# Kernel optimization log

Measured on AMD Instinct MI355X. Metric: run time of the kernel, lower is better.

Reference implementation:

```python
import jax, jax.numpy as jnp
import numpy as np

K_TOP = 32
TEMPERATURE = 0.1
EPS = 1e-12  # torch F.normalize eps


def _l2_normalize(x):
    n = jnp.linalg.norm(x, axis=-1, keepdims=True)
    return x / jnp.maximum(n, EPS)


def setup_inputs() -> dict:
    key = jax.random.key(0)
    kq, kk, kv = jax.random.split(key, 3)
    B, T, d_k, d_v, N = 4, 512, 512, 512, 65536
    queries = jax.random.normal(kq, (B, T, d_k), dtype=jnp.float32)
    keys = jax.random.normal(kk, (N, d_k), dtype=jnp.float32)
    values = jax.random.normal(kv, (N, d_v), dtype=jnp.float32)
    return {"queries": queries, "keys": keys, "values": values}


def reference(queries, keys, values):
    B, T, d_k = queries.shape
    d_v = values.shape[1]
    flat_q = queries.reshape(B * T, d_k)
    qn = _l2_normalize(flat_q)           # [BT, d_k]
    kn = _l2_normalize(keys)             # [N, d_k]
    scores = qn @ kn.T                   # [BT, N] cosine similarities
    topk_scores, topk_idx = jax.lax.top_k(scores, K_TOP)  # [BT, K]
    attn = jax.nn.softmax(topk_scores / TEMPERATURE, axis=-1)  # [BT, K]
    retrieved = values[topk_idx]         # [BT, K, d_v]
    aggregated = jnp.einsum('nk,nkd->nd', attn, retrieved)  # [BT, d_v]
    return (aggregated.reshape(B, T, d_v),
            attn.reshape(B, T, K_TOP),
            topk_idx.reshape(B, T, K_TOP))
```

## Files before the change

kernel.cpp:

```cpp
#include <hip/hip_runtime.h>
#include <math.h>

#define M_ROWS 2048
#define N_KEYS 65536
#define DKK 512
#define DVV 512
#define KTOP 32
#define NSPLIT 16
#define NRANGE (N_KEYS / NSPLIT)
#define BM 128
#define BN 128
#define MBLKS (M_ROWS / BM)
#define NTILES (NRANGE / BN)
#define KSTEPS (DKK / 32)
#define TOT (NTILES * KSTEPS)
#define CAP 16
#define CSTR 17

typedef _Float16 f16x8 __attribute__((ext_vector_type(8)));
typedef _Float16 f16x4v __attribute__((ext_vector_type(4)));
typedef float f32x4 __attribute__((ext_vector_type(4)));


__device__ __forceinline__ void split4(const float4 v, float inv,
                                       _Float16* ph, _Float16* pl) {
  f16x4v h, l;
  float y;
  y = v.x * inv; h[0] = (_Float16)y; l[0] = (_Float16)(y - (float)h[0]);
  y = v.y * inv; h[1] = (_Float16)y; l[1] = (_Float16)(y - (float)h[1]);
  y = v.z * inv; h[2] = (_Float16)y; l[2] = (_Float16)(y - (float)h[2]);
  y = v.w * inv; h[3] = (_Float16)y; l[3] = (_Float16)(y - (float)h[3]);
  *(f16x4v*)ph = h; *(f16x4v*)pl = l;
}

__global__ void __launch_bounds__(256) norm_split_kernel(
    const float* __restrict__ q, const float* __restrict__ keys,
    _Float16* __restrict__ Qh, _Float16* __restrict__ Ql,
    _Float16* __restrict__ Kh, _Float16* __restrict__ Kl) {
  const int gw = (blockIdx.x * 256 + threadIdx.x) >> 6;
  const int lane = threadIdx.x & 63;
  const float* row; _Float16 *oh, *ol;
  if (gw < M_ROWS) {
    row = q + (size_t)gw * DKK; oh = Qh + (size_t)gw * DKK; ol = Ql + (size_t)gw * DKK;
  } else {
    const int n = gw - M_ROWS;
    if (n >= N_KEYS) return;
    row = keys + (size_t)n * DKK; oh = Kh + (size_t)n * DKK; ol = Kl + (size_t)n * DKK;
  }
  const float4 a = ((const float4*)row)[lane];
  const float4 b = ((const float4*)row)[lane + 64];
  float s = a.x*a.x + a.y*a.y + a.z*a.z + a.w*a.w
          + b.x*b.x + b.y*b.y + b.z*b.z + b.w*b.w;
#pragma unroll
  for (int off = 32; off; off >>= 1) s += __shfl_xor(s, off);
  const float inv = 1.0f / fmaxf(sqrtf(s), 1e-12f);
  split4(a, inv, oh + lane * 4,       ol + lane * 4);
  split4(b, inv, oh + 256 + lane * 4, ol + 256 + lane * 4);
}

__device__ __forceinline__ void insert32(float* tS, int* tI, float s, int idx) {
  const float ms = tS[31]; const int mi_ = tI[31];
  if (s < ms || (s == ms && idx > mi_)) return;
  int p = 0;
  while (p < KTOP && (tS[p] > s || (tS[p] == s && tI[p] < idx))) ++p;
  for (int qq = KTOP - 1; qq > p; --qq) { tS[qq] = tS[qq-1]; tI[qq] = tI[qq-1]; }
  tS[p] = s; tI[p] = idx;
}

__device__ __forceinline__ void gll16(const _Float16* g, _Float16* l) {
  __builtin_amdgcn_global_load_lds(
      (const __attribute__((address_space(1))) void*)g,
      (__attribute__((address_space(3))) void*)l, 16, 0, 0);
}

#define STAGE(B, N0V, KOF) do {                                  \
  const size_t _qa = qsrc + (size_t)(KOF);                       \
  const size_t _ba = (size_t)(N0V) * DKK + bsrc + (size_t)(KOF); \
  gll16(Qh + _qa, &stA[B][0][ldsA]);                             \
  gll16(Ql + _qa, &stA[B][1][ldsA]);                             \
  gll16(Kh + _ba, &stB[B][0][ldsA]);                             \
  gll16(Kl + _ba, &stB[B][1][ldsA]);                             \
} while (0)

#define KBAR(NVM) do {                                           \
  __builtin_amdgcn_sched_barrier(0);                             \
  asm volatile("s_waitcnt vmcnt(" #NVM ")" ::: "memory");        \
  __builtin_amdgcn_sched_barrier(0);                             \
  __builtin_amdgcn_s_barrier();                                  \
  __builtin_amdgcn_sched_barrier(0);                             \
} while (0)

#define LBAR() do {                                              \
  __builtin_amdgcn_sched_barrier(0);                             \
  asm volatile("s_waitcnt lgkmcnt(0)" ::: "memory");             \
  __builtin_amdgcn_sched_barrier(0);                             \
  __builtin_amdgcn_s_barrier();                                  \
  __builtin_amdgcn_sched_barrier(0);                             \
} while (0)

__global__ void __launch_bounds__(512, 2) gemm_topk_kernel(
    const _Float16* __restrict__ Qh, const _Float16* __restrict__ Ql,
    const _Float16* __restrict__ Kh, const _Float16* __restrict__ Kl,
    float* __restrict__ pscore, int* __restrict__ pidx) {
  __shared__ __attribute__((aligned(16))) _Float16 stA[3][2][BM * 32];
  __shared__ __attribute__((aligned(16))) _Float16 stB[3][2][BN * 32];
  __shared__ float topS[BM * 33];
  __shared__ int   topI[BM * 33];
  __shared__ float candS[BM * CSTR];
  __shared__ int   candI[BM * CSTR];
  __shared__ float mS[BM];
  __shared__ int   cnt[BM];
  __shared__ int   sOver;

  const int tid  = threadIdx.x;
  const int lane = tid & 63;
  const int w    = tid >> 6;
  const int wr   = w >> 1, wc = w & 1;
  const int cl   = lane & 15;
  const int g    = lane >> 4;
  const int g4   = g * 4;

  const int lin   = (int)(blockIdx.x + gridDim.x * blockIdx.y);
  const int virt  = (lin & 7) * 32 + (lin >> 3);
  const int mblk  = virt & (MBLKS - 1);
  const int split = virt >> 4;
  const int qbase  = mblk * BM;
  const int nbase0 = split * NRANGE;

  const int soct = (tid & 3) ^ ((tid >> 3) & 3);
  const int ldsA = tid * 8;
  const size_t qsrc = (size_t)(qbase + (tid >> 2)) * DKK + (size_t)soct * 8;
  const size_t bsrc = (size_t)(tid >> 2) * DKK + (size_t)soct * 8;

  int offA[2], offB[4];
#pragma unroll
  for (int mi = 0; mi < 2; ++mi) {
    const int r = wr * 32 + mi * 16 + cl;
    offA[mi] = r * 32 + (g ^ ((r >> 1) & 3)) * 8;
  }
#pragma unroll
  for (int ni = 0; ni < 4; ++ni) {
    const int c = wc * 64 + ni * 16 + cl;
    offB[ni] = c * 32 + (g ^ ((c >> 1) & 3)) * 8;
  }

  if (tid < BM) {
    mS[tid] = -INFINITY; cnt[tid] = 0;
#pragma unroll
    for (int j = 0; j < KTOP; ++j) { topS[tid*33+j] = -INFINITY; topI[tid*33+j] = 0x7fffffff; }
  }
  if (tid == 0) sOver = 0;

  STAGE(0, nbase0, 0);
  STAGE(1, nbase0, 32);

  int cur = 0;

  for (int ct = 0; ct < NTILES; ++ct) {
    const int n0 = nbase0 + ct * BN;
    f32x4 acc[2][4];
#pragma unroll
    for (int mi = 0; mi < 2; ++mi)
#pragma unroll
      for (int ni = 0; ni < 4; ++ni) acc[mi][ni] = (f32x4)0.0f;

    for (int ks = 0; ks < KSTEPS; ++ks) {
      const int s = ct * KSTEPS + ks;
      if (s == TOT - 1) { KBAR(0); } else { KBAR(4); }

      if (s + 2 < TOT) {
        int b2 = cur + 2; if (b2 >= 3) b2 -= 3;
        const int s2 = s + 2;
        const int ct2 = s2 >> 4, ks2 = s2 & 15;
        STAGE(b2, nbase0 + ct2 * BN, ks2 * 32);
      }

      f16x8 Ah[2], Al[2], Bh[4], Bl[4];
#pragma unroll
      for (int mi = 0; mi < 2; ++mi) {
        Ah[mi] = *(const f16x8*)&stA[cur][0][offA[mi]];
        Al[mi] = *(const f16x8*)&stA[cur][1][offA[mi]];
      }
#pragma unroll
      for (int ni = 0; ni < 4; ++ni) {
        Bh[ni] = *(const f16x8*)&stB[cur][0][offB[ni]];
        Bl[ni] = *(const f16x8*)&stB[cur][1][offB[ni]];
      }
      __builtin_amdgcn_s_setprio(1);
#pragma unroll
      for (int mi = 0; mi < 2; ++mi)
#pragma unroll
        for (int ni = 0; ni < 4; ++ni) {
          acc[mi][ni] = __builtin_amdgcn_mfma_f32_16x16x32_f16(Al[mi], Bh[ni], acc[mi][ni], 0, 0, 0);
          acc[mi][ni] = __builtin_amdgcn_mfma_f32_16x16x32_f16(Ah[mi], Bl[ni], acc[mi][ni], 0, 0, 0);
          acc[mi][ni] = __builtin_amdgcn_mfma_f32_16x16x32_f16(Ah[mi], Bh[ni], acc[mi][ni], 0, 0, 0);
        }
      __builtin_amdgcn_s_setprio(0);

      ++cur; if (cur >= 3) cur -= 3;
    }

    LBAR();
    float m[2][4];
#pragma unroll
    for (int mi = 0; mi < 2; ++mi) {
      const f32x4 mv = *(const f32x4*)&mS[wr * 32 + mi * 16 + g4];
      m[mi][0] = mv[0]; m[mi][1] = mv[1]; m[mi][2] = mv[2]; m[mi][3] = mv[3];
    }
    unsigned int pend = 0u;
#pragma unroll
    for (int mi = 0; mi < 2; ++mi)
#pragma unroll
      for (int ni = 0; ni < 4; ++ni)
#pragma unroll
        for (int j = 0; j < 4; ++j)
          if (acc[mi][ni][j] >= m[mi][j])
            pend |= 1u << (mi * 16 + ni * 4 + j);

    for (;;) {
      if (pend) {
#pragma unroll
        for (int mi = 0; mi < 2; ++mi)
#pragma unroll
          for (int ni = 0; ni < 4; ++ni)
#pragma unroll
            for (int j = 0; j < 4; ++j) {
              const int bit = mi * 16 + ni * 4 + j;
              if (pend & (1u << bit)) {
                const int r = wr * 32 + mi * 16 + g4 + j;
                const int t = atomicAdd(&cnt[r], 1);
                if (t < CAP) {
                  candS[r * CSTR + t] = acc[mi][ni][j];
                  candI[r * CSTR + t] = n0 + wc * 64 + ni * 16 + cl;
                  pend &= ~(1u << bit);
                }
              }
            }
      }
      LBAR();
      if (tid < BM) {
        int nc = cnt[tid];
        if (nc > CAP) { sOver = 1; nc = CAP; }
        float* tS = &topS[tid * 33];
        int*   tI = &topI[tid * 33];
        for (int e = 0; e < nc; ++e) insert32(tS, tI, candS[tid * CSTR + e], candI[tid * CSTR + e]);
        mS[tid] = tS[KTOP - 1];
        cnt[tid] = 0;
      }
      LBAR();
      const int over = sOver;
      LBAR();
      if (tid == 0) sOver = 0;
      if (!over) break;
#pragma unroll
      for (int mi = 0; mi < 2; ++mi) {
        const f32x4 mv = *(const f32x4*)&mS[wr * 32 + mi * 16 + g4];
        m[mi][0] = mv[0]; m[mi][1] = mv[1]; m[mi][2] = mv[2]; m[mi][3] = mv[3];
      }
      unsigned int keep = 0u;
#pragma unroll
      for (int mi = 0; mi < 2; ++mi)
#pragma unroll
        for (int ni = 0; ni < 4; ++ni)
#pragma unroll
          for (int j = 0; j < 4; ++j) {
            const int bit = mi * 16 + ni * 4 + j;
            if ((pend & (1u << bit)) && acc[mi][ni][j] >= m[mi][j])
              keep |= 1u << bit;
          }
      pend = keep;
    }
  }

  if (tid < BM) {
    const size_t base = ((size_t)(qbase + tid) * NSPLIT + split) * KTOP;
    for (int j = 0; j < KTOP; ++j) {
      pscore[base + j] = topS[tid * 33 + j];
      pidx[base + j]   = topI[tid * 33 + j];
    }
  }
}


#define QB 128
#define NB 128
#define KC 32
#define FNTILES (NRANGE / NB)
#define KCH (DKK / KC)
#define LDST 132

__global__ void __launch_bounds__(256) norm_kernel(
    const float* __restrict__ q, const float* __restrict__ keys,
    float* __restrict__ qn, float* __restrict__ kinv) {
  const int gw = (blockIdx.x * 256 + threadIdx.x) >> 6;
  const int lane = threadIdx.x & 63;
  if (gw < M_ROWS) {
    const float* row = q + (size_t)gw * DKK;
    float4 a = ((const float4*)row)[lane];
    float4 b = ((const float4*)row)[lane + 64];
    float s = a.x*a.x + a.y*a.y + a.z*a.z + a.w*a.w
            + b.x*b.x + b.y*b.y + b.z*b.z + b.w*b.w;
#pragma unroll
    for (int off = 32; off; off >>= 1) s += __shfl_xor(s, off);
    const float inv = 1.0f / fmaxf(sqrtf(s), 1e-12f);
    float* orow = qn + (size_t)gw * DKK;
    ((float4*)orow)[lane]      = make_float4(a.x*inv, a.y*inv, a.z*inv, a.w*inv);
    ((float4*)orow)[lane + 64] = make_float4(b.x*inv, b.y*inv, b.z*inv, b.w*inv);
  } else {
    const int n = gw - M_ROWS;
    if (n < N_KEYS) {
      const float* row = keys + (size_t)n * DKK;
      float4 a = ((const float4*)row)[lane];
      float4 b = ((const float4*)row)[lane + 64];
      float s = a.x*a.x + a.y*a.y + a.z*a.z + a.w*a.w
              + b.x*b.x + b.y*b.y + b.z*b.z + b.w*b.w;
#pragma unroll
      for (int off = 32; off; off >>= 1) s += __shfl_xor(s, off);
      if (lane == 0) kinv[n] = 1.0f / fmaxf(sqrtf(s), 1e-12f);
    }
  }
}

__device__ __forceinline__ void lds_wr_tile(float* dst, int k8, int r, float4 v, float scale) {
  dst[(k8 * 4 + 0) * LDST + r] = v.x * scale;
  dst[(k8 * 4 + 1) * LDST + r] = v.y * scale;
  dst[(k8 * 4 + 2) * LDST + r] = v.z * scale;
  dst[(k8 * 4 + 3) * LDST + r] = v.w * scale;
}

__global__ void __launch_bounds__(256, 1) score_topk_kernel(
    const float* __restrict__ qn, const float* __restrict__ keys,
    const float* __restrict__ kinv,
    float* __restrict__ pscore, int* __restrict__ pidx) {
  __shared__ float u[16896];
  __shared__ float topS[QB * KTOP];
  __shared__ int   topI[QB * KTOP];

  const int tid = threadIdx.x;
  const int tx = tid & 15, ty = tid >> 4;
  const int qbase = blockIdx.y * QB;
  const int nbase0 = blockIdx.x * NRANGE;

  for (int i = tid; i < QB * KTOP; i += 256) { topS[i] = -INFINITY; topI[i] = 0; }
  __syncthreads();

  for (int t = 0; t < FNTILES; ++t) {
    const int n0 = nbase0 + t * NB;
    float acc[8][8];
#pragma unroll
    for (int i = 0; i < 8; ++i)
#pragma unroll
      for (int j = 0; j < 8; ++j) acc[i][j] = 0.0f;

#pragma unroll
    for (int p = 0; p < 4; ++p) {
      const int id = tid + p * 256;
      const int r = id >> 3, k8 = id & 7;
      const float4 va = *(const float4*)&qn[(size_t)(qbase + r) * DKK + k8 * 4];
      const float4 vb = *(const float4*)&keys[(size_t)(n0 + r) * DKK + k8 * 4];
      const float kv = kinv[n0 + r];
      lds_wr_tile(u, k8, r, va, 1.0f);
      lds_wr_tile(u + 4224, k8, r, vb, kv);
    }
    __syncthreads();

    for (int kc = 0; kc < KCH; ++kc) {
      float4 pa[4], pb[4]; float pk[4];
      const bool pre = (kc + 1 < KCH);
      if (pre) {
#pragma unroll
        for (int p = 0; p < 4; ++p) {
          const int id = tid + p * 256;
          const int r = id >> 3, k8 = id & 7;
          pa[p] = *(const float4*)&qn[(size_t)(qbase + r) * DKK + (kc + 1) * KC + k8 * 4];
          pb[p] = *(const float4*)&keys[(size_t)(n0 + r) * DKK + (kc + 1) * KC + k8 * 4];
          pk[p] = kinv[n0 + r];
        }
      }
      const float* As = u + (kc & 1) * 8448;
      const float* Bs = As + 4224;
#pragma unroll 4
      for (int kk = 0; kk < KC; ++kk) {
        const float4 a0 = *(const float4*)&As[kk * LDST + ty * 4];
        const float4 a1 = *(const float4*)&As[kk * LDST + ty * 4 + 64];
        const float4 b0 = *(const float4*)&Bs[kk * LDST + tx * 4];
        const float4 b1 = *(const float4*)&Bs[kk * LDST + tx * 4 + 64];
        const float av[8] = {a0.x,a0.y,a0.z,a0.w,a1.x,a1.y,a1.z,a1.w};
        const float bv[8] = {b0.x,b0.y,b0.z,b0.w,b1.x,b1.y,b1.z,b1.w};
#pragma unroll
        for (int i = 0; i < 8; ++i)
#pragma unroll
          for (int j = 0; j < 8; ++j)
            acc[i][j] = fmaf(av[i], bv[j], acc[i][j]);
      }
      if (pre) {
        float* Ad = u + ((kc + 1) & 1) * 8448;
        float* Bd = Ad + 4224;
#pragma unroll
        for (int p = 0; p < 4; ++p) {
          const int id = tid + p * 256;
          const int r = id >> 3, k8 = id & 7;
          lds_wr_tile(Ad, k8, r, pa[p], 1.0f);
          lds_wr_tile(Bd, k8, r, pb[p], pk[p]);
        }
      }
      __syncthreads();
    }

#pragma unroll
    for (int ib = 0; ib < 2; ++ib)
#pragma unroll
      for (int i = 0; i < 4; ++i) {
        const int r = ty * 4 + i + ib * 64;
#pragma unroll
        for (int jb = 0; jb < 2; ++jb) {
          *(float4*)&u[r * LDST + tx * 4 + jb * 64] =
              make_float4(acc[ib*4+i][jb*4+0], acc[ib*4+i][jb*4+1],
                          acc[ib*4+i][jb*4+2], acc[ib*4+i][jb*4+3]);
        }
      }
    __syncthreads();

    if (tid < QB) {
      const int row = tid;
      float* tS = &topS[row * KTOP];
      int*   tI = &topI[row * KTOP];
      float mSv = tS[KTOP - 1]; int mIv = tI[KTOP - 1];
      for (int c4 = 0; c4 < NB / 4; ++c4) {
        const float4 v = *(const float4*)&u[row * LDST + c4 * 4];
#pragma unroll
        for (int wv = 0; wv < 4; ++wv) {
          const float s = (&v.x)[wv];
          const int idx = n0 + c4 * 4 + wv;
          if (s > mSv || (s == mSv && idx < mIv)) {
            int p = 0;
            while (p < KTOP && (tS[p] > s || (tS[p] == s && tI[p] < idx))) ++p;
            for (int qq = KTOP - 1; qq > p; --qq) { tS[qq] = tS[qq-1]; tI[qq] = tI[qq-1]; }
            tS[p] = s; tI[p] = idx;
            mSv = tS[KTOP - 1]; mIv = tI[KTOP - 1];
          }
        }
      }
    }
    __syncthreads();
  }

  if (tid < QB) {
    const size_t base = ((size_t)(qbase + tid) * NSPLIT + blockIdx.x) * KTOP;
    for (int j = 0; j < KTOP; ++j) {
      pscore[base + j] = topS[tid * KTOP + j];
      pidx[base + j]   = topI[tid * KTOP + j];
    }
  }
}

__global__ void __launch_bounds__(256) merge_kernel(
    const float* __restrict__ pscore, const int* __restrict__ pidx,
    const float* __restrict__ values,
    float* __restrict__ out_agg, float* __restrict__ out_attn, float* __restrict__ out_idx) {
  __shared__ float attn_s[KTOP];
  __shared__ int   sel_i[KTOP];
  const int row = blockIdx.x;
  const int tid = threadIdx.x;

  if (tid < 64) {
    const int lane = tid;
    const float* ps = pscore + (size_t)row * NSPLIT * KTOP;
    const int*   pi = pidx   + (size_t)row * NSPLIT * KTOP;
    int pos = 0;
    float s; int idx;
    if (lane < NSPLIT) { s = ps[lane * KTOP]; idx = pi[lane * KTOP]; }
    else { s = -INFINITY; idx = 0x7fffffff; }
    for (int it = 0; it < KTOP; ++it) {
      float wsv = s; int wi = idx; int wl = lane;
#pragma unroll
      for (int off = 32; off; off >>= 1) {
        const float os = __shfl_xor(wsv, off);
        const int   oi = __shfl_xor(wi, off);
        const int   ol = __shfl_xor(wl, off);
        if (os > wsv || (os == wsv && oi < wi)) { wsv = os; wi = oi; wl = ol; }
      }
      if (lane == 0) { attn_s[it] = wsv; sel_i[it] = wi; }
      if (lane == wl) {
        ++pos;
        if (pos < KTOP) { s = ps[lane * KTOP + pos]; idx = pi[lane * KTOP + pos]; }
        else { s = -INFINITY; idx = 0x7fffffff; }
      }
    }
  }
  __syncthreads();
  if (tid < KTOP) {
    const float mm = attn_s[0];
    const float e = expf((attn_s[tid] - mm) * 10.0f);
    float tsum = e;
#pragma unroll
    for (int off = 16; off; off >>= 1) tsum += __shfl_xor(tsum, off);
    const float a = e / tsum;
    out_attn[(size_t)row * KTOP + tid] = a;
    out_idx [(size_t)row * KTOP + tid] = (float)sel_i[tid];
    attn_s[tid] = a;
  }
  __syncthreads();

  const int d = tid * 2;
  float2 accv = make_float2(0.0f, 0.0f);
  for (int j = 0; j < KTOP; ++j) {
    const float wgt = attn_s[j];
    const float2 v = *(const float2*)&values[(size_t)sel_i[j] * DVV + d];
    accv.x = fmaf(wgt, v.x, accv.x);
    accv.y = fmaf(wgt, v.y, accv.y);
  }
  *(float2*)&out_agg[(size_t)row * DVV + d] = accv;
}

extern "C" void kernel_launch(void* const* d_in, const int* in_sizes, int n_in,
                              void* d_out, int out_size, void* d_ws, size_t ws_size,
                              hipStream_t stream) {
  const float* q      = (const float*)d_in[0];
  const float* keys   = (const float*)d_in[1];
  const float* values = (const float*)d_in[2];

  float* out      = (float*)d_out;
  float* out_agg  = out;
  float* out_attn = out + (size_t)M_ROWS * DVV;
  float* out_idx  = out_attn + (size_t)M_ROWS * KTOP;

  const size_t needFast =
      (size_t)M_ROWS * DKK * 2 * 2
    + (size_t)N_KEYS * DKK * 2 * 2
    + (size_t)M_ROWS * NSPLIT * KTOP * 8;

  if (ws_size >= needFast) {
    _Float16* Qh = (_Float16*)d_ws;
    _Float16* Ql = Qh + (size_t)M_ROWS * DKK;
    _Float16* Kh = Ql + (size_t)M_ROWS * DKK;
    _Float16* Kl = Kh + (size_t)N_KEYS * DKK;
    float* pscore = (float*)(Kl + (size_t)N_KEYS * DKK);
    int*   pidx   = (int*)(pscore + (size_t)M_ROWS * NSPLIT * KTOP);

    norm_split_kernel<<<(M_ROWS + N_KEYS) / 4, 256, 0, stream>>>(q, keys, Qh, Ql, Kh, Kl);
    dim3 g2(MBLKS, NSPLIT, 1);
    gemm_topk_kernel<<<g2, 512, 0, stream>>>(Qh, Ql, Kh, Kl, pscore, pidx);
    merge_kernel<<<M_ROWS, 256, 0, stream>>>(pscore, pidx, values, out_agg, out_attn, out_idx);
  } else {
    float* ws     = (float*)d_ws;
    float* qn     = ws;
    float* kinv   = qn + (size_t)M_ROWS * DKK;
    float* pscore = kinv + N_KEYS;
    int*   pidx   = (int*)(pscore + (size_t)M_ROWS * NSPLIT * KTOP);

    norm_kernel<<<(M_ROWS + N_KEYS) / 4, 256, 0, stream>>>(q, keys, qn, kinv);
    dim3 g2(NSPLIT, M_ROWS / QB, 1);
    score_topk_kernel<<<g2, 256, 0, stream>>>(qn, keys, kinv, pscore, pidx);
    merge_kernel<<<M_ROWS, 256, 0, stream>>>(pscore, pidx, values, out_agg, out_attn, out_idx);
  }
}
```

Baseline: 1.797 ms.

## Pre-tile swizzled fp16 operands and keep Q-high fragments in registers

```diff
diff --git a/kernel.cpp b/kernel.cpp
--- a/kernel.cpp
+++ b/kernel.cpp
@@ -16,46 +16,51 @@
 #define TOT (NTILES * KSTEPS)
 #define CAP 16
 #define CSTR 17
+#define TILE_E 4096
 
 typedef _Float16 f16x8 __attribute__((ext_vector_type(8)));
-typedef _Float16 f16x4v __attribute__((ext_vector_type(4)));
 typedef float f32x4 __attribute__((ext_vector_type(4)));
 
-
-__device__ __forceinline__ void split4(const float4 v, float inv,
-                                       _Float16* ph, _Float16* pl) {
-  f16x4v h, l;
-  float y;
-  y = v.x * inv; h[0] = (_Float16)y; l[0] = (_Float16)(y - (float)h[0]);
-  y = v.y * inv; h[1] = (_Float16)y; l[1] = (_Float16)(y - (float)h[1]);
-  y = v.z * inv; h[2] = (_Float16)y; l[2] = (_Float16)(y - (float)h[2]);
-  y = v.w * inv; h[3] = (_Float16)y; l[3] = (_Float16)(y - (float)h[3]);
-  *(f16x4v*)ph = h; *(f16x4v*)pl = l;
-}
 
 __global__ void __launch_bounds__(256) norm_split_kernel(
     const float* __restrict__ q, const float* __restrict__ keys,
-    _Float16* __restrict__ Qh, _Float16* __restrict__ Ql,
-    _Float16* __restrict__ Kh, _Float16* __restrict__ Kl) {
+    _Float16* __restrict__ QhT, _Float16* __restrict__ QlT,
+    _Float16* __restrict__ KhT, _Float16* __restrict__ KlT) {
   const int gw = (blockIdx.x * 256 + threadIdx.x) >> 6;
   const int lane = threadIdx.x & 63;
-  const float* row; _Float16 *oh, *ol;
+  const float* row; _Float16 *oh, *ol; int rr;
   if (gw < M_ROWS) {
-    row = q + (size_t)gw * DKK; oh = Qh + (size_t)gw * DKK; ol = Ql + (size_t)gw * DKK;
+    row = q + (size_t)gw * DKK; rr = gw & 127;
+    const size_t tb = (size_t)(gw >> 7) * 16 * TILE_E;
+    oh = QhT + tb; ol = QlT + tb;
   } else {
     const int n = gw - M_ROWS;
     if (n >= N_KEYS) return;
-    row = keys + (size_t)n * DKK; oh = Kh + (size_t)n * DKK; ol = Kl + (size_t)n * DKK;
-  }
-  const float4 a = ((const float4*)row)[lane];
-  const float4 b = ((const float4*)row)[lane + 64];
+    row = keys + (size_t)n * DKK; rr = n & 127;
+    const size_t tb = (size_t)(n >> 7) * 16 * TILE_E;
+    oh = KhT + tb; ol = KlT + tb;
+  }
+  const float4 a = *(const float4*)&row[lane * 8];
+  const float4 b = *(const float4*)&row[lane * 8 + 4];
   float s = a.x*a.x + a.y*a.y + a.z*a.z + a.w*a.w
           + b.x*b.x + b.y*b.y + b.z*b.z + b.w*b.w;
 #pragma unroll
   for (int off = 32; off; off >>= 1) s += __shfl_xor(s, off);
   const float inv = 1.0f / fmaxf(sqrtf(s), 1e-12f);
-  split4(a, inv, oh + lane * 4,       ol + lane * 4);
-  split4(b, inv, oh + 256 + lane * 4, ol + 256 + lane * 4);
+
+  f16x8 h, l;
+  const float e[8] = {a.x, a.y, a.z, a.w, b.x, b.y, b.z, b.w};
+#pragma unroll
+  for (int j = 0; j < 8; ++j) {
+    const float y = e[j] * inv;
+    h[j] = (_Float16)y;
+    l[j] = (_Float16)(y - (float)h[j]);
+  }
+  const int ks = lane >> 2, oct = lane & 3;
+  const int po = oct ^ ((rr >> 1) & 3);
+  const size_t off = (size_t)ks * TILE_E + rr * 32 + po * 8;
+  *(f16x8*)&oh[off] = h;
+  *(f16x8*)&ol[off] = l;
 }
 
 __device__ __forceinline__ void insert32(float* tS, int* tI, float s, int idx) {
@@ -73,37 +78,67 @@
       (__attribute__((address_space(3))) void*)l, 16, 0, 0);
 }
 
-#define STAGE(B, N0V, KOF) do {                                  \
-  const size_t _qa = qsrc + (size_t)(KOF);                       \
-  const size_t _ba = (size_t)(N0V) * DKK + bsrc + (size_t)(KOF); \
-  gll16(Qh + _qa, &stA[B][0][ldsA]);                             \
-  gll16(Ql + _qa, &stA[B][1][ldsA]);                             \
-  gll16(Kh + _ba, &stB[B][0][ldsA]);                             \
-  gll16(Kl + _ba, &stB[B][1][ldsA]);                             \
+#define SQL(i) sQl##i
+#define SKH(i) sKh##i
+#define SKL(i) sKl##i
+
+#define STAGE(B, KB, KS2) do {                                         \
+  gll16(QlT + qlb + (size_t)(KS2) * TILE_E, &SQL(B)[ldsA]);            \
+  gll16(KhT + (KB) + (size_t)(KS2) * TILE_E, &SKH(B)[ldsA]);           \
+  gll16(KlT + (KB) + (size_t)(KS2) * TILE_E, &SKL(B)[ldsA]);           \
 } while (0)
 
-#define KBAR(NVM) do {                                           \
-  __builtin_amdgcn_sched_barrier(0);                             \
-  asm volatile("s_waitcnt vmcnt(" #NVM ")" ::: "memory");        \
-  __builtin_amdgcn_sched_barrier(0);                             \
-  __builtin_amdgcn_s_barrier();                                  \
-  __builtin_amdgcn_sched_barrier(0);                             \
+#define KBAR(NVM) do {                                                 \
+  __builtin_amdgcn_sched_barrier(0);                                   \
+  asm volatile("s_waitcnt vmcnt(" #NVM ")" ::: "memory");              \
+  __builtin_amdgcn_sched_barrier(0);                                   \
+  __builtin_amdgcn_s_barrier();                                        \
+  __builtin_amdgcn_sched_barrier(0);                                   \
 } while (0)
 
-#define LBAR() do {                                              \
-  __builtin_amdgcn_sched_barrier(0);                             \
-  asm volatile("s_waitcnt lgkmcnt(0)" ::: "memory");             \
-  __builtin_amdgcn_sched_barrier(0);                             \
-  __builtin_amdgcn_s_barrier();                                  \
-  __builtin_amdgcn_sched_barrier(0);                             \
+#define LBAR() do {                                                    \
+  __builtin_amdgcn_sched_barrier(0);                                   \
+  asm volatile("s_waitcnt lgkmcnt(0)" ::: "memory");                   \
+  __builtin_amdgcn_sched_barrier(0);                                   \
+  __builtin_amdgcn_s_barrier();                                        \
+  __builtin_amdgcn_sched_barrier(0);                                   \
 } while (0)
 
+#define ONESTEP(KS, RB, SB) do {                                       \
+  if (lastct && (KS) == 14) { KBAR(3); }                               \
+  else if (lastct && (KS) == 15) { KBAR(0); }                          \
+  else { KBAR(6); }                                                    \
+  if ((KS) < 13) { STAGE(SB, kb, (KS) + 3); }                          \
+  else if (!lastct) { STAGE(SB, kb + 16 * TILE_E, (KS) - 13); }        \
+  f16x8 Al_[2], Bh_[4], Bl_[4];                                        \
+  Al_[0] = *(const f16x8*)&SQL(RB)[offA[0]];                           \
+  Al_[1] = *(const f16x8*)&SQL(RB)[offA[1]];                           \
+  _Pragma("unroll")                                                    \
+  for (int ni = 0; ni < 4; ++ni) {                                     \
+    Bh_[ni] = *(const f16x8*)&SKH(RB)[offB[ni]];                       \
+    Bl_[ni] = *(const f16x8*)&SKL(RB)[offB[ni]];                       \
+  }                                                                    \
+  __builtin_amdgcn_s_setprio(1);                                       \
+  _Pragma("unroll")                                                    \
+  for (int mi = 0; mi < 2; ++mi) {                                     \
+    const f16x8 qa = (mi == 0) ? qh0[KS] : qh1[KS];                    \
+    _Pragma("unroll")                                                  \
+    for (int ni = 0; ni < 4; ++ni) {                                   \
+      acc[mi][ni] = __builtin_amdgcn_mfma_f32_16x16x32_f16(Al_[mi], Bh_[ni], acc[mi][ni], 0, 0, 0); \
+      acc[mi][ni] = __builtin_amdgcn_mfma_f32_16x16x32_f16(qa, Bl_[ni], acc[mi][ni], 0, 0, 0);      \
+      acc[mi][ni] = __builtin_amdgcn_mfma_f32_16x16x32_f16(qa, Bh_[ni], acc[mi][ni], 0, 0, 0);      \
+    }                                                                  \
+  }                                                                    \
+  __builtin_amdgcn_s_setprio(0);                                       \
+} while (0)
+
 __global__ void __launch_bounds__(512, 2) gemm_topk_kernel(
-    const _Float16* __restrict__ Qh, const _Float16* __restrict__ Ql,
-    const _Float16* __restrict__ Kh, const _Float16* __restrict__ Kl,
+    const _Float16* __restrict__ QhT, const _Float16* __restrict__ QlT,
+    const _Float16* __restrict__ KhT, const _Float16* __restrict__ KlT,
     float* __restrict__ pscore, int* __restrict__ pidx) {
-  __shared__ __attribute__((aligned(16))) _Float16 stA[3][2][BM * 32];
-  __shared__ __attribute__((aligned(16))) _Float16 stB[3][2][BN * 32];
+  __shared__ __attribute__((aligned(16))) _Float16 sQl0[TILE_E], sQl1[TILE_E], sQl2[TILE_E], sQl3[TILE_E];
+  __shared__ __attribute__((aligned(16))) _Float16 sKh0[TILE_E], sKh1[TILE_E], sKh2[TILE_E], sKh3[TILE_E];
+  __shared__ __attribute__((aligned(16))) _Float16 sKl0[TILE_E], sKl1[TILE_E], sKl2[TILE_E], sKl3[TILE_E];
   __shared__ float topS[BM * 33];
   __shared__ int   topI[BM * 33];
   __shared__ float candS[BM * CSTR];
@@ -127,10 +162,9 @@
   const int qbase  = mblk * BM;
   const int nbase0 = split * NRANGE;
 
-  const int soct = (tid & 3) ^ ((tid >> 3) & 3);
   const int ldsA = tid * 8;
-  const size_t qsrc = (size_t)(qbase + (tid >> 2)) * DKK + (size_t)soct * 8;
-  const size_t bsrc = (size_t)(tid >> 2) * DKK + (size_t)soct * 8;
+  const size_t qlb = (size_t)mblk * 16 * TILE_E + ldsA;
+  const size_t kb0 = (size_t)(split * NTILES) * 16 * TILE_E + ldsA;
 
   int offA[2], offB[4];
 #pragma unroll
@@ -144,6 +178,16 @@
     offB[ni] = c * 32 + (g ^ ((c >> 1) & 3)) * 8;
   }
 
+  f16x8 qh0[16], qh1[16];
+  {
+    const size_t qhb = (size_t)mblk * 16 * TILE_E;
+#pragma unroll
+    for (int ks = 0; ks < 16; ++ks) {
+      qh0[ks] = *(const f16x8*)&QhT[qhb + (size_t)ks * TILE_E + offA[0]];
+      qh1[ks] = *(const f16x8*)&QhT[qhb + (size_t)ks * TILE_E + offA[1]];
+    }
+  }
+
   if (tid < BM) {
     mS[tid] = -INFINITY; cnt[tid] = 0;
 #pragma unroll
@@ -151,12 +195,13 @@
   }
   if (tid == 0) sOver = 0;
 
-  STAGE(0, nbase0, 0);
-  STAGE(1, nbase0, 32);
-
-  int cur = 0;
+  STAGE(0, kb0, 0);
+  STAGE(1, kb0, 1);
+  STAGE(2, kb0, 2);
 
   for (int ct = 0; ct < NTILES; ++ct) {
+    const bool lastct = (ct == NTILES - 1);
+    const size_t kb = kb0 + (size_t)ct * 16 * TILE_E;
     const int n0 = nbase0 + ct * BN;
     f32x4 acc[2][4];
 #pragma unroll
@@ -164,41 +209,10 @@
 #pragma unroll
       for (int ni = 0; ni < 4; ++ni) acc[mi][ni] = (f32x4)0.0f;
 
-    for (int ks = 0; ks < KSTEPS; ++ks) {
-      const int s = ct * KSTEPS + ks;
-      if (s == TOT - 1) { KBAR(0); } else { KBAR(4); }
-
-      if (s + 2 < TOT) {
-        int b2 = cur + 2; if (b2 >= 3) b2 -= 3;
-        const int s2 = s + 2;
-        const int ct2 = s2 >> 4, ks2 = s2 & 15;
-        STAGE(b2, nbase0 + ct2 * BN, ks2 * 32);
-      }
-
-      f16x8 Ah[2], Al[2], Bh[4], Bl[4];
-#pragma unroll
-      for (int mi = 0; mi < 2; ++mi) {
-        Ah[mi] = *(const f16x8*)&stA[cur][0][offA[mi]];
-        Al[mi] = *(const f16x8*)&stA[cur][1][offA[mi]];
-      }
-#pragma unroll
-      for (int ni = 0; ni < 4; ++ni) {
-        Bh[ni] = *(const f16x8*)&stB[cur][0][offB[ni]];
-        Bl[ni] = *(const f16x8*)&stB[cur][1][offB[ni]];
-      }
-      __builtin_amdgcn_s_setprio(1);
-#pragma unroll
-      for (int mi = 0; mi < 2; ++mi)
-#pragma unroll
-        for (int ni = 0; ni < 4; ++ni) {
-          acc[mi][ni] = __builtin_amdgcn_mfma_f32_16x16x32_f16(Al[mi], Bh[ni], acc[mi][ni], 0, 0, 0);
-          acc[mi][ni] = __builtin_amdgcn_mfma_f32_16x16x32_f16(Ah[mi], Bl[ni], acc[mi][ni], 0, 0, 0);
-          acc[mi][ni] = __builtin_amdgcn_mfma_f32_16x16x32_f16(Ah[mi], Bh[ni], acc[mi][ni], 0, 0, 0);
-        }
-      __builtin_amdgcn_s_setprio(0);
-
-      ++cur; if (cur >= 3) cur -= 3;
-    }
+    ONESTEP(0, 0, 3);  ONESTEP(1, 1, 0);  ONESTEP(2, 2, 1);  ONESTEP(3, 3, 2);
+    ONESTEP(4, 0, 3);  ONESTEP(5, 1, 0);  ONESTEP(6, 2, 1);  ONESTEP(7, 3, 2);
+    ONESTEP(8, 0, 3);  ONESTEP(9, 1, 0);  ONESTEP(10, 2, 1); ONESTEP(11, 3, 2);
+    ONESTEP(12, 0, 3); ONESTEP(13, 1, 0); ONESTEP(14, 2, 1); ONESTEP(15, 3, 2);
 
     LBAR();
     float m[2][4];
@@ -531,16 +545,16 @@
     + (size_t)M_ROWS * NSPLIT * KTOP * 8;
 
   if (ws_size >= needFast) {
-    _Float16* Qh = (_Float16*)d_ws;
-    _Float16* Ql = Qh + (size_t)M_ROWS * DKK;
-    _Float16* Kh = Ql + (size_t)M_ROWS * DKK;
-    _Float16* Kl = Kh + (size_t)N_KEYS * DKK;
-    float* pscore = (float*)(Kl + (size_t)N_KEYS * DKK);
+    _Float16* QhT = (_Float16*)d_ws;
+    _Float16* QlT = QhT + (size_t)M_ROWS * DKK;
+    _Float16* KhT = QlT + (size_t)M_ROWS * DKK;
+    _Float16* KlT = KhT + (size_t)N_KEYS * DKK;
+    float* pscore = (float*)(KlT + (size_t)N_KEYS * DKK);
     int*   pidx   = (int*)(pscore + (size_t)M_ROWS * NSPLIT * KTOP);
 
-    norm_split_kernel<<<(M_ROWS + N_KEYS) / 4, 256, 0, stream>>>(q, keys, Qh, Ql, Kh, Kl);
+    norm_split_kernel<<<(M_ROWS + N_KEYS) / 4, 256, 0, stream>>>(q, keys, QhT, QlT, KhT, KlT);
     dim3 g2(MBLKS, NSPLIT, 1);
-    gemm_topk_kernel<<<g2, 512, 0, stream>>>(Qh, Ql, Kh, Kl, pscore, pidx);
+    gemm_topk_kernel<<<g2, 512, 0, stream>>>(QhT, QlT, KhT, KlT, pscore, pidx);
     merge_kernel<<<M_ROWS, 256, 0, stream>>>(pscore, pidx, values, out_agg, out_attn, out_idx);
   } else {
     float* ws     = (float*)d_ws;
```

After: 1.928 ms. 7.3% more time.
